# Kernel tuning notes

Measured on AMD Instinct MI355X. Metric: run time of the kernel, lower is better.

## Reference

```python
import jax, jax.numpy as jnp
import numpy as np

B, N, T = 512, 24, 25
IN, L, H, OUT = 8, 64, 256, 128


def quat_mul(q, r):
    w1, x1, y1, z1 = jnp.split(q, 4, -1)
    w2, x2, y2, z2 = jnp.split(r, 4, -1)
    return jnp.concatenate([
        w1 * w2 - x1 * x2 - y1 * y2 - z1 * z2,
        w1 * x2 + x1 * w2 + y1 * z2 - z1 * y2,
        w1 * y2 - x1 * z2 + y1 * w2 + z1 * x2,
        w1 * z2 + x1 * y2 - y1 * x2 + z1 * w2], -1)


def node_linear(x, W, b, G):
    # per-node weights [N,F,O], then graph-influence mixing G[N,N]
    y = jnp.einsum('bnf,nfo->bno', x, W) + b
    return jnp.einsum('mn,bno->bmo', G, y)


def graph_linear(x, W, b, G):
    # shared weights [F,O], then graph-influence mixing
    y = jnp.einsum('bnf,fo->bno', x, W) + b
    return jnp.einsum('mn,bno->bmo', G, y)


def lstm_step(x, h, c, Wx, Wh, b, G):
    gates = jnp.einsum('bnf,nfo->bno', x, Wx) + jnp.einsum('bnf,nfo->bno', h, Wh) + b
    gates = jnp.einsum('mn,bno->bmo', G, gates)
    i, f, g, o = jnp.split(gates, 4, -1)
    c = jax.nn.sigmoid(f) * c + jax.nn.sigmoid(i) * jnp.tanh(g)
    h = jax.nn.sigmoid(o) * jnp.tanh(c)
    return h, c


def _p(key, shape, scale):
    return jax.random.normal(key, shape, jnp.float32) * scale


def setup_inputs() -> dict:
    key = jax.random.key(0)
    ks = jax.random.split(key, 20)
    in0 = L + IN
    inp = {
        'x': jax.random.normal(ks[0], (B, 1, N, IN), jnp.float32),
        'enc': jax.random.normal(ks[1], (B, 1, N, H), jnp.float32),
        'z': jax.random.normal(ks[2], (B, 1, N, L), jnp.float32),
        'y': jax.random.normal(ks[3], (B, T, N, 4), jnp.float32),
        'G': jnp.eye(N, dtype=jnp.float32) + 0.02 * jax.random.normal(ks[4], (N, N), jnp.float32),
        'Wx0': _p(ks[5], (N, in0, 4 * OUT), in0 ** -0.5),
        'Wh0': _p(ks[6], (N, OUT, 4 * OUT), OUT ** -0.5),
        'b0': jnp.zeros((N, 4 * OUT), jnp.float32),
        'Wx1': _p(ks[7], (N, OUT, 4 * OUT), OUT ** -0.5),
        'Wh1': _p(ks[8], (N, OUT, 4 * OUT), OUT ** -0.5),
        'b1': jnp.zeros((N, 4 * OUT), jnp.float32),
        'fc_W': _p(ks[9], (N, OUT, OUT), OUT ** -0.5),
        'fc_b': jnp.zeros((N, OUT), jnp.float32),
        'fc2_W': _p(ks[10], (N, OUT, OUT), OUT ** -0.5),
        'fc2_b': jnp.zeros((N, OUT), jnp.float32),
        'ih1_W': _p(ks[11], (H, OUT), H ** -0.5),
        'ih1_b': jnp.zeros((OUT,), jnp.float32),
        'ih2_W': _p(ks[12], (H, OUT), H ** -0.5),
        'ih2_b': jnp.zeros((OUT,), jnp.float32),
        'loc_W': _p(ks[13], (OUT, 3), OUT ** -0.5),
        'loc_b': jnp.zeros((3,), jnp.float32),
        'logz_W': _p(ks[14], (OUT, 4), OUT ** -0.5),
        'logz_b': jnp.zeros((4,), jnp.float32),
    }
    return inp


def reference(x, enc, z, y, G, Wx0, Wh0, b0, Wx1, Wh1, b1, fc_W, fc_b, fc2_W, fc2_b,
              ih1_W, ih1_b, ih2_W, ih2_b, loc_W, loc_b, logz_W, logz_b):
    # eval mode: dropout = identity, no teacher forcing (y unused); rnn2/xi2 are dead code.
    xs, zs, encs = x[:, 0], z[:, 0], enc[:, 0]          # [B,N,*]
    h0 = graph_linear(encs, ih1_W, ih1_b, G)            # shared initial h for both layers
    c0 = graph_linear(encs, ih2_W, ih2_b, G)            # shared initial c for both layers
    loc_start0 = xs[..., :4]
    xi0 = jnp.concatenate([zs, xs], -1)                 # [B,N,L+IN]

    def step(carry, _):
        xi, loc_start, h1, c1, h2, c2 = carry
        h1, c1 = lstm_step(xi, h1, c1, Wx0, Wh0, b0, G)
        h2, c2 = lstm_step(h1, h2, c2, Wx1, Wh1, b1, G)
        yi = jnp.tanh(h2)
        yi1 = jnp.tanh(node_linear(yi, fc_W, fc_b, G))
        yi2 = jnp.tanh(node_linear(yi, fc2_W, fc2_b, G))
        loc3 = graph_linear(yi1, loc_W, loc_b, G)       # [B,N,3]
        log_Z = graph_linear(yi2, logz_W, logz_b, G)    # [B,N,4]
        w = jnp.ones(loc3.shape[:-1] + (1,), loc3.dtype)
        loc4 = jnp.concatenate([w, loc3], -1)
        loc_d = loc4 * jax.lax.rsqrt(jnp.sum(loc4 * loc4, -1, keepdims=True))  # validate
        loc = quat_mul(loc_start, loc_d)                # state_representation.sum
        xi_next = jnp.concatenate([zs, loc, loc_d], -1)
        return (xi_next, loc, h1, c1, h2, c2), (loc, log_Z)

    _, (locs, logzs) = jax.lax.scan(step, (xi0, loc_start0, h0, c0, h0, c0), None, length=T)
    out = jnp.moveaxis(locs, 0, 1)[:, :, None]          # [B,T,1,N,4]
    out_log_diag = jnp.moveaxis(logzs, 0, 1)[:, :, None]
    return out, out_log_diag
```

## Files before the change

kernel.cpp:

```cpp
#include <hip/hip_runtime.h>
#include <math.h>

#define Bsz 512
#define Nn  24
#define Tt  25

typedef _Float16 f16;
typedef _Float16 f16x8 __attribute__((ext_vector_type(8)));
typedef _Float16 f16x4 __attribute__((ext_vector_type(4)));
typedef float f32x4 __attribute__((ext_vector_type(4)));

__global__ __launch_bounds__(256) void gemm128(
    const f16* __restrict__ Act, const float* __restrict__ Act32, int Ka,
    const f16* __restrict__ W, size_t wstride, int otiles, int bpn,
    const float* __restrict__ bias, int bstride,
    f16* __restrict__ Y, int ystride, int yoff)
{
    const int bid = blockIdx.x;
    const int n     = (bid & 7) + 8 * (bid / (8 * bpn));
    const int inner = (bid >> 3) % bpn;
    const int o0 = (inner % otiles) * 128;
    const int b0 = (inner / otiles) * 128;
    const int tid  = threadIdx.x;
    const int wave = tid >> 6, lane = tid & 63;
    const int wm = (wave >> 1) * 64;
    const int wn = (wave & 1) * 64;
    const int m16 = lane & 15, quad = lane >> 4;

    __shared__ __attribute__((aligned(16))) f16 sW[128][72];
    __shared__ __attribute__((aligned(16))) f16 sB[128][72];

    const f16* Wn = W + (size_t)n * wstride;
    f32x4 acc[4][4] = {};
    const int r = tid >> 3, cc = (tid & 7) * 8;

    for (int k0 = 0; k0 < Ka; k0 += 64) {
        for (int row = r; row < 128; row += 32)
            *(f16x8*)&sW[row][cc] = *(const f16x8*)&Wn[(size_t)(o0 + row) * Ka + k0 + cc];
        if (Act) {
            for (int row = r; row < 128; row += 32)
                *(f16x8*)&sB[row][cc] = *(const f16x8*)&Act[((size_t)(b0 + row) * Nn + n) * Ka + k0 + cc];
        } else {
            for (int row = r; row < 128; row += 32) {
                const float* src = &Act32[((size_t)(b0 + row) * Nn + n) * Ka + k0 + cc];
                f16x8 v;
#pragma unroll
                for (int u = 0; u < 8; u++) v[u] = (f16)src[u];
                *(f16x8*)&sB[row][cc] = v;
            }
        }
        __syncthreads();
#pragma unroll
        for (int kk = 0; kk < 64; kk += 32) {
            f16x8 af[4], bf[4];
#pragma unroll
            for (int i = 0; i < 4; i++)
                af[i] = *(const f16x8*)&sW[wm + i * 16 + m16][kk + quad * 8];
#pragma unroll
            for (int j = 0; j < 4; j++)
                bf[j] = *(const f16x8*)&sB[wn + j * 16 + m16][kk + quad * 8];
#pragma unroll
            for (int i = 0; i < 4; i++)
#pragma unroll
                for (int j = 0; j < 4; j++)
                    acc[i][j] = __builtin_amdgcn_mfma_f32_16x16x32_f16(af[i], bf[j], acc[i][j], 0, 0, 0);
        }
        __syncthreads();
    }
#pragma unroll
    for (int i = 0; i < 4; i++) {
        const int orow = o0 + wm + i * 16 + quad * 4;
        float4 bv = make_float4(0.f, 0.f, 0.f, 0.f);
        if (bias) bv = *(const float4*)&bias[(size_t)n * bstride + orow];
#pragma unroll
        for (int j = 0; j < 4; j++) {
            const int bcol = b0 + wn + j * 16 + m16;
            size_t yi = ((size_t)bcol * Nn + n) * (size_t)ystride + yoff + orow;
            f16x4 o4;
            o4[0] = (f16)(acc[i][j][0] + bv.x);
            o4[1] = (f16)(acc[i][j][1] + bv.y);
            o4[2] = (f16)(acc[i][j][2] + bv.z);
            o4[3] = (f16)(acc[i][j][3] + bv.w);
            *(f16x4*)&Y[yi] = o4;
        }
    }
}

__global__ __launch_bounds__(256) void prep_w01(
    const float* __restrict__ Wx0, const float* __restrict__ Wh0,
    const float* __restrict__ Wx1, const float* __restrict__ Wh1,
    f16* __restrict__ Wz, f16* __restrict__ W2ext, f16* __restrict__ W8,
    f16* __restrict__ Wh0t)
{
    size_t idx = (size_t)blockIdx.x * 256 + threadIdx.x;
    const size_t nz = (size_t)Nn * 512 * 64;
    const size_t n2 = (size_t)Nn * 1024 * 256;
    const size_t n8 = (size_t)Nn * 8 * 512;
    const size_t nh = (size_t)Nn * 512 * 128;
    if (idx < nz) {
        int k = idx & 63; int o = (idx >> 6) & 511; int n = (int)(idx >> 15);
        Wz[idx] = (f16)Wx0[((size_t)n * 72 + k) * 512 + o];
    } else if (idx < nz + n2) {
        size_t i3 = idx - nz;
        int k = (int)(i3 & 255);
        size_t no = i3 >> 8;
        int o = (int)(no & 1023); int n = (int)(no >> 10);
        float v;
        if (o < 512) v = (k < 128) ? Wx1[((size_t)n * 128 + k) * 512 + o]
                                   : Wh1[((size_t)n * 128 + (k - 128)) * 512 + o];
        else         v = (k < 128) ? Wh0[((size_t)n * 128 + k) * 512 + (o - 512)] : 0.f;
        W2ext[i3] = (f16)v;
    } else if (idx < nz + n2 + n8) {
        size_t i4 = idx - nz - n2;
        int o = (int)(i4 & 511);
        size_t ko = i4 >> 9;
        int k = (int)(ko & 7); int n = (int)(ko >> 3);
        W8[i4] = (f16)Wx0[((size_t)n * 72 + 64 + k) * 512 + o];
    } else if (idx < nz + n2 + n8 + nh) {
        size_t i5 = idx - nz - n2 - n8;
        int k = (int)(i5 & 127);
        size_t no = i5 >> 7;
        int o = (int)(no & 511); int n = (int)(no >> 9);
        Wh0t[i5] = (f16)Wh0[((size_t)n * 128 + k) * 512 + o];
    }
}

__global__ __launch_bounds__(256) void prep_wf(
    const float* __restrict__ fcW, const float* __restrict__ fc2W,
    f16* __restrict__ Wtf)
{
    size_t idx = (size_t)blockIdx.x * 256 + threadIdx.x;
    if (idx >= (size_t)Nn * 256 * 128) return;
    int k = (int)(idx & 127);
    size_t no = idx >> 7;
    int o = (int)(no & 255); int n = (int)(no >> 8);
    float v = (o < 128) ? fcW[((size_t)n * 128 + k) * 128 + o]
                        : fc2W[((size_t)n * 128 + k) * 128 + (o - 128)];
    Wtf[idx] = (f16)v;
}

__global__ __launch_bounds__(256) void prep_wi(
    const float* __restrict__ ih1W, const float* __restrict__ ih2W,
    const float* __restrict__ ih1b, const float* __restrict__ ih2b,
    const float* __restrict__ fcb, const float* __restrict__ fc2b,
    const float* __restrict__ b1,
    f16* __restrict__ Wti, float* __restrict__ bi, float* __restrict__ bcat,
    float* __restrict__ bcat2)
{
    int idx = blockIdx.x * 256 + threadIdx.x;
    int k = idx & 255, o = idx >> 8;
    Wti[idx] = (f16)((o < 128) ? ih1W[(size_t)k * 128 + o] : ih2W[(size_t)k * 128 + (o - 128)]);
    if (idx < 256) bi[idx] = (idx < 128) ? ih1b[idx] : ih2b[idx - 128];
    if (idx < Nn * 256) {
        int n = idx >> 8, oo = idx & 255;
        bcat[idx] = (oo < 128) ? fcb[n * 128 + oo] : fc2b[n * 128 + (oo - 128)];
    }
    if (idx < Nn * 1024) {
        int n = idx >> 10, oo = idx & 1023;
        bcat2[idx] = (oo < 512) ? b1[n * 512 + oo] : 0.f;
    }
}

__global__ __launch_bounds__(256) void init_small(
    const float* __restrict__ x, f16* __restrict__ v8f, float* __restrict__ ls)
{
    size_t idx = (size_t)blockIdx.x * 256 + threadIdx.x;
    if (idx < (size_t)Bsz * Nn * 8) {
        v8f[idx] = (f16)x[idx];
        if ((idx & 7) < 4) {
            size_t bn = idx >> 3;
            ls[bn * 4 + (idx & 3)] = x[idx];
        }
    }
}

__global__ __launch_bounds__(256) void mix_init(
    const f16* __restrict__ Yhc, const float* __restrict__ G,
    f16* __restrict__ h0f, f16* __restrict__ l2cat,
    float* __restrict__ c1, float* __restrict__ c2)
{
    const int b = blockIdx.x;
    const int tid = threadIdx.x;
    __shared__ float sY[6144], sG[576];
    for (int i = tid; i < 576; i += 256) sG[i] = G[i];
    for (int v = tid; v < 768; v += 256) {
        int c8 = (v & 31) * 8, n = v >> 5;
        f16x8 t = *(const f16x8*)&Yhc[((size_t)b * Nn + n) * 256 + c8];
        float* d = &sY[n * 256 + c8];
#pragma unroll
        for (int u = 0; u < 8; u++) d[u] = (float)t[u];
    }
    __syncthreads();
    for (int w = tid; w < 3072; w += 256) {
        int o = w & 127, m = w >> 7;
        float ah = 0.f, ac = 0.f;
#pragma unroll
        for (int n = 0; n < 24; n++) {
            float g = sG[m * 24 + n];
            ah += g * sY[n * 256 + o];
            ac += g * sY[n * 256 + 128 + o];
        }
        size_t row = (size_t)b * Nn + m;
        f16 hf = (f16)ah;
        h0f[row * 128 + o] = hf;
        l2cat[row * 256 + 128 + o] = hf;
        c1[row * 128 + o] = ac;
        c2[row * 128 + o] = ac;
    }
}

__global__ __launch_bounds__(256) void mix1c(
    const f16* __restrict__ ypB, const f16* __restrict__ base1,
    const f16* __restrict__ W8, const f16* __restrict__ v8f,
    const float* __restrict__ G,
    float* __restrict__ c1, f16* __restrict__ l2cat)
{
    const int bg = blockIdx.x >> 2;
    const int jt = (blockIdx.x & 3) * 32;
    const int b0 = bg * 8;
    const int tid = threadIdx.x;
    __shared__ __attribute__((aligned(16))) f16 sYc[8][24][136];
    __shared__ float sG[576];
    __shared__ __attribute__((aligned(16))) f16 sV8[8][24][8];
    for (int i = tid; i < 576; i += 256) sG[i] = G[i];
    for (int i = tid; i < 192; i += 256) {
        int bb = i / 24, n = i - bb * 24;
        *(f16x8*)&sV8[bb][n][0] = *(const f16x8*)&v8f[((size_t)(b0 + bb) * Nn + n) * 8];
    }
    __syncthreads();
    for (int i = tid; i < 3072; i += 256) {
        const int c8 = (i & 15) * 8;
        const int n  = (i >> 4) % 24;
        const int bb = (i >> 4) / 24;
        const int g = c8 >> 5;
        const int o8 = g * 128 + jt + (c8 & 31);
        const size_t rowb = (size_t)(b0 + bb) * Nn + n;
        f16x8 pp = *(const f16x8*)&ypB[rowb * 1024 + 512 + o8];
        f16x8 bs = *(const f16x8*)&base1[rowb * 512 + o8];
        float acc[8];
#pragma unroll
        for (int u = 0; u < 8; u++) acc[u] = (float)pp[u] + (float)bs[u];
#pragma unroll
        for (int k = 0; k < 8; k++) {
            float v = (float)sV8[bb][n][k];
            f16x8 ww = *(const f16x8*)&W8[((size_t)n * 8 + k) * 512 + o8];
#pragma unroll
            for (int u = 0; u < 8; u++) acc[u] += v * (float)ww[u];
        }
        f16x8 oo;
#pragma unroll
        for (int u = 0; u < 8; u++) oo[u] = (f16)acc[u];
        *(f16x8*)&sYc[bb][n][c8] = oo;
    }
    __syncthreads();
    for (int w = tid; w < 1536; w += 256) {
        const int j4 = (w & 7) * 4;
        const int m  = (w >> 3) % 24;
        const int bb = (w >> 3) / 24;
        float gi[4] = {}, gf[4] = {}, gg[4] = {}, go[4] = {};
        const float* gr = &sG[m * 24];
#pragma unroll
        for (int n = 0; n < 24; n++) {
            float g = gr[n];
            const f16* yn = &sYc[bb][n][0];
            f16x4 vi = *(const f16x4*)&yn[j4];
            f16x4 vf = *(const f16x4*)&yn[32 + j4];
            f16x4 vg = *(const f16x4*)&yn[64 + j4];
            f16x4 vo = *(const f16x4*)&yn[96 + j4];
#pragma unroll
            for (int u = 0; u < 4; u++) {
                gi[u] += g * (float)vi[u];
                gf[u] += g * (float)vf[u];
                gg[u] += g * (float)vg[u];
                go[u] += g * (float)vo[u];
            }
        }
        const size_t row = (size_t)(b0 + bb) * Nn + m;
        const int col = jt + j4;
        float cv[4];
        *(float4*)cv = *(const float4*)&c1[row * 128 + col];
        f16x4 ha;
#pragma unroll
        for (int u = 0; u < 4; u++) {
            float si = 1.f / (1.f + expf(-gi[u]));
            float sf = 1.f / (1.f + expf(-gf[u]));
            float so = 1.f / (1.f + expf(-go[u]));
            float cn = sf * cv[u] + si * tanhf(gg[u]);
            cv[u] = cn;
            ha[u] = (f16)(so * tanhf(cn));
        }
        *(float4*)&c1[row * 128 + col] = *(float4*)cv;
        *(f16x4*)&l2cat[row * 256 + col] = ha;
    }
}

__global__ __launch_bounds__(256) void mix2(
    const f16* __restrict__ ypB, const float* __restrict__ G,
    float* __restrict__ c,
    f16* __restrict__ dstA, f16* __restrict__ dstB)
{
    const int b = blockIdx.x;
    const int tid = threadIdx.x;
    __shared__ __attribute__((aligned(16))) f16 sY[12288];
    __shared__ float sG[576];
    for (int i = tid; i < 576; i += 256) sG[i] = G[i];
    for (int i = tid; i < 1536; i += 256) {
        int n = i >> 6, c8 = (i & 63) * 8;
        *(f16x8*)&sY[n * 512 + c8] = *(const f16x8*)&ypB[((size_t)b * Nn + n) * 1024 + c8];
    }
    __syncthreads();
    for (int w = tid; w < 768; w += 256) {
        const int m = w >> 5, j4 = (w & 31) * 4;
        float gi[4] = {}, gf[4] = {}, gg[4] = {}, go[4] = {};
        const float* gr = &sG[m * 24];
#pragma unroll
        for (int n = 0; n < 24; n++) {
            float g = gr[n];
            const f16* yn = &sY[n * 512];
            f16x4 vi = *(const f16x4*)&yn[j4];
            f16x4 vf = *(const f16x4*)&yn[128 + j4];
            f16x4 vg = *(const f16x4*)&yn[256 + j4];
            f16x4 vo = *(const f16x4*)&yn[384 + j4];
#pragma unroll
            for (int u = 0; u < 4; u++) {
                gi[u] += g * (float)vi[u];
                gf[u] += g * (float)vf[u];
                gg[u] += g * (float)vg[u];
                go[u] += g * (float)vo[u];
            }
        }
        const size_t row = (size_t)b * Nn + m;
        float cv[4];
        *(float4*)cv = *(const float4*)&c[row * 128 + j4];
        f16x4 ha, hb;
#pragma unroll
        for (int u = 0; u < 4; u++) {
            float si = 1.f / (1.f + expf(-gi[u]));
            float sf = 1.f / (1.f + expf(-gf[u]));
            float so = 1.f / (1.f + expf(-go[u]));
            float cn = sf * cv[u] + si * tanhf(gg[u]);
            cv[u] = cn;
            float h = so * tanhf(cn);
            ha[u] = (f16)h;
            hb[u] = (f16)tanhf(h);
        }
        *(float4*)&c[row * 128 + j4] = *(float4*)cv;
        *(f16x4*)&dstA[row * 256 + 128 + j4] = ha;
        *(f16x4*)&dstB[row * 128 + j4] = hb;
    }
}

__global__ __launch_bounds__(256) void finstep(
    const f16* __restrict__ p, const float* __restrict__ G,
    const float* __restrict__ locW, const float* __restrict__ locb,
    const float* __restrict__ lzW, const float* __restrict__ lzb,
    float* __restrict__ ls, f16* __restrict__ v8f,
    float* __restrict__ out, int t)
{
    const int b = blockIdx.x;
    const int tid = threadIdx.x;
    __shared__ __attribute__((aligned(16))) f16 sP[6144];
    __shared__ __attribute__((aligned(16))) f16 sY1[3072], sY2[3072];
    __shared__ float sG[576];
    __shared__ float sLp[24][3], sZp[24][4], sL3[24][3], sZ3[24][4];
    for (int i = tid; i < 576; i += 256) sG[i] = G[i];
    for (int i = tid; i < 768; i += 256) {
        int n = i >> 5, c8 = (i & 31) * 8;
        *(f16x8*)&sP[n * 256 + c8] = *(const f16x8*)&p[((size_t)b * Nn + n) * 256 + c8];
    }
    __syncthreads();
    for (int w = tid; w < 768; w += 256) {
        const int m = w >> 5, o4 = (w & 31) * 4;
        float a1[4] = {}, a2[4] = {};
        const float* gr = &sG[m * 24];
#pragma unroll
        for (int n = 0; n < 24; n++) {
            float g = gr[n];
            f16x4 p1 = *(const f16x4*)&sP[n * 256 + o4];
            f16x4 p2 = *(const f16x4*)&sP[n * 256 + 128 + o4];
#pragma unroll
            for (int u = 0; u < 4; u++) { a1[u] += g * (float)p1[u]; a2[u] += g * (float)p2[u]; }
        }
        f16x4 y1, y2;
#pragma unroll
        for (int u = 0; u < 4; u++) { y1[u] = (f16)tanhf(a1[u]); y2[u] = (f16)tanhf(a2[u]); }
        *(f16x4*)&sY1[m * 128 + o4] = y1;
        *(f16x4*)&sY2[m * 128 + o4] = y2;
    }
    __syncthreads();
    if (tid < 72) {
        int m = tid / 3, j = tid - m * 3;
        float s = locb[j];
        for (int o = 0; o < 128; o++) s += (float)sY1[m * 128 + o] * locW[o * 3 + j];
        sLp[m][j] = s;
    } else if (tid < 168) {
        int w2 = tid - 72; int m = w2 >> 2, j = w2 & 3;
        float s = lzb[j];
        for (int o = 0; o < 128; o++) s += (float)sY2[m * 128 + o] * lzW[o * 4 + j];
        sZp[m][j] = s;
    }
    __syncthreads();
    if (tid < 72) {
        int m = tid / 3, j = tid - m * 3;
        float s = 0.f;
#pragma unroll
        for (int n = 0; n < 24; n++) s += sG[m * 24 + n] * sLp[n][j];
        sL3[m][j] = s;
    } else if (tid < 168) {
        int w2 = tid - 72; int m = w2 >> 2, j = w2 & 3;
        float s = 0.f;
#pragma unroll
        for (int n = 0; n < 24; n++) s += sG[m * 24 + n] * sZp[n][j];
        sZ3[m][j] = s;
    }
    __syncthreads();
    if (tid < 24) {
        const int m = tid;
        float xx = sL3[m][0], xy = sL3[m][1], xz = sL3[m][2];
        float r = rsqrtf(1.f + xx * xx + xy * xy + xz * xz);
        float dw = r, dx = xx * r, dy = xy * r, dz = xz * r;
        size_t li = ((size_t)b * Nn + m) * 4;
        float qw = ls[li], qx = ls[li + 1], qy = ls[li + 2], qz = ls[li + 3];
        float lw = qw * dw - qx * dx - qy * dy - qz * dz;
        float lx = qw * dx + qx * dw + qy * dz - qz * dy;
        float ly = qw * dy - qx * dz + qy * dw + qz * dx;
        float lz = qw * dz + qx * dy - qy * dx + qz * dw;
        size_t oi = (((size_t)b * Tt + t) * Nn + m) * 4;
        out[oi + 0] = lw; out[oi + 1] = lx; out[oi + 2] = ly; out[oi + 3] = lz;
        size_t zi = (size_t)Bsz * Tt * Nn * 4 + oi;
        out[zi + 0] = sZ3[m][0]; out[zi + 1] = sZ3[m][1];
        out[zi + 2] = sZ3[m][2]; out[zi + 3] = sZ3[m][3];
        ls[li] = lw; ls[li + 1] = lx; ls[li + 2] = ly; ls[li + 3] = lz;
        f16x8 v8;
        v8[0] = (f16)lw; v8[1] = (f16)lx; v8[2] = (f16)ly; v8[3] = (f16)lz;
        v8[4] = (f16)dw; v8[5] = (f16)dx; v8[6] = (f16)dy; v8[7] = (f16)dz;
        *(f16x8*)&v8f[((size_t)b * Nn + m) * 8] = v8;
    }
}

extern "C" void kernel_launch(void* const* d_in, const int* in_sizes, int n_in,
                              void* d_out, int out_size, void* d_ws, size_t ws_size,
                              hipStream_t stream)
{
    const float* x    = (const float*)d_in[0];
    const float* enc  = (const float*)d_in[1];
    const float* z    = (const float*)d_in[2];
    const float* G    = (const float*)d_in[4];
    const float* Wx0  = (const float*)d_in[5];
    const float* Wh0  = (const float*)d_in[6];
    const float* b0i  = (const float*)d_in[7];
    const float* Wx1  = (const float*)d_in[8];
    const float* Wh1  = (const float*)d_in[9];
    const float* b1i  = (const float*)d_in[10];
    const float* fcW  = (const float*)d_in[11];
    const float* fcb  = (const float*)d_in[12];
    const float* fc2W = (const float*)d_in[13];
    const float* fc2b = (const float*)d_in[14];
    const float* ih1W = (const float*)d_in[15];
    const float* ih1b = (const float*)d_in[16];
    const float* ih2W = (const float*)d_in[17];
    const float* ih2b = (const float*)d_in[18];
    const float* locW = (const float*)d_in[19];
    const float* locb = (const float*)d_in[20];
    const float* lzW  = (const float*)d_in[21];
    const float* lzb  = (const float*)d_in[22];
    float* out = (float*)d_out;

    const size_t BN = (size_t)Bsz * Nn;
    char* wp = (char*)d_ws;
    size_t off = 0;
    auto carve = [&](size_t bytes) -> char* {
        char* pc = wp + off;
        off += (bytes + 255) & ~(size_t)255;
        return pc;
    };
    f16*   Wz     = (f16*)carve((size_t)Nn * 512 * 64 * 2);
    f16*   W2ext  = (f16*)carve((size_t)Nn * 1024 * 256 * 2);
    f16*   W8     = (f16*)carve((size_t)Nn * 8 * 512 * 2);
    f16*   Wh0t   = (f16*)carve((size_t)Nn * 512 * 128 * 2);
    f16*   Wtf    = (f16*)carve((size_t)Nn * 256 * 128 * 2);
    f16*   Wti    = (f16*)carve((size_t)256 * 256 * 2);
    float* bcat   = (float*)carve((size_t)Nn * 256 * 4);
    float* bcat2  = (float*)carve((size_t)Nn * 1024 * 4);
    float* bi     = (float*)carve(256 * 4);
    f16*   base1  = (f16*)carve(BN * 512 * 2);
    f16*   l2cat  = (f16*)carve(BN * 256 * 2);
    f16*   yib    = (f16*)carve(BN * 128 * 2);
    f16*   h0f    = (f16*)carve(BN * 128 * 2);
    float* c1     = (float*)carve(BN * 128 * 4);
    float* c2     = (float*)carve(BN * 128 * 4);
    float* ls     = (float*)carve(BN * 4 * 4);
    f16*   v8f    = (f16*)carve(BN * 8 * 2);
    f16*   ypB    = (f16*)carve(BN * 1024 * 2);
    f16*   yp0    = (f16*)carve(BN * 256 * 2);
    f16*   pbuf   = (f16*)carve(BN * 256 * 2);

    prep_w01<<<34176, 256, 0, stream>>>(Wx0, Wh0, Wx1, Wh1, Wz, W2ext, W8, Wh0t);
    prep_wf<<<3072, 256, 0, stream>>>(fcW, fc2W, Wtf);
    prep_wi<<<256, 256, 0, stream>>>(ih1W, ih2W, ih1b, ih2b, fcb, fc2b, b1i,
                                     Wti, bi, bcat, bcat2);
    init_small<<<384, 256, 0, stream>>>(x, v8f, ls);

    gemm128<<<384, 256, 0, stream>>>(nullptr, z, 64, Wz, (size_t)512 * 64, 4, 16,
                                     b0i, 512, base1, 512, 0);
    gemm128<<<192, 256, 0, stream>>>(nullptr, enc, 256, Wti, 0, 2, 8,
                                     bi, 0, yp0, 256, 0);
    mix_init<<<512, 256, 0, stream>>>(yp0, G, h0f, l2cat, c1, c2);
    gemm128<<<384, 256, 0, stream>>>(h0f, nullptr, 128, Wh0t, (size_t)512 * 128, 4, 16,
                                     nullptr, 0, ypB, 1024, 512);

    for (int t = 0; t < Tt; t++) {
        mix1c<<<256, 256, 0, stream>>>(ypB, base1, W8, v8f, G, c1, l2cat);
        gemm128<<<768, 256, 0, stream>>>(l2cat, nullptr, 256, W2ext, (size_t)1024 * 256,
                                         8, 32, bcat2, 1024, ypB, 1024, 0);
        mix2<<<512, 256, 0, stream>>>(ypB, G, c2, l2cat, yib);
        gemm128<<<192, 256, 0, stream>>>(yib, nullptr, 128, Wtf, (size_t)256 * 128,
                                         2, 8, bcat, 256, pbuf, 256, 0);
        finstep<<<512, 256, 0, stream>>>(pbuf, G, locW, locb, lzW, lzb, ls, v8f, out, t);
    }
}
```

Before: 2.698 ms.

## Fold z-projection into recurrent GEMM by extending K to 320 and tiled weight prep

The constant z input is appended to the activation buffer (l2cat now 320 wide), and the matching Wx0 rows are added to the Wh0 half of the extended weight. This removes the separate base1 precompute and its per-step load in mix1c, and the layer-0 bias moves into bcat2. Weight-prep kernels are rewritten as tiled shared-memory transposes for coalesced access, and the initial h0 GEMM reuses the extended weights. In exchange, every per-step GEMM does 25% more K work, including a Wx1/Wh1 half that multiplies the z columns by zero weights.

```diff
diff --git a/kernel.cpp b/kernel.cpp
--- a/kernel.cpp
+++ b/kernel.cpp
@@ -12,14 +12,14 @@
 
 __global__ __launch_bounds__(256) void gemm128(
     const f16* __restrict__ Act, const float* __restrict__ Act32, int Ka,
-    const f16* __restrict__ W, size_t wstride, int otiles, int bpn,
+    const f16* __restrict__ W, size_t wstride, int otiles, int bpn, int obase,
     const float* __restrict__ bias, int bstride,
-    f16* __restrict__ Y, int ystride, int yoff)
+    f16* __restrict__ Y, int ystride)
 {
     const int bid = blockIdx.x;
     const int n     = (bid & 7) + 8 * (bid / (8 * bpn));
     const int inner = (bid >> 3) % bpn;
-    const int o0 = (inner % otiles) * 128;
+    const int o0 = obase + (inner % otiles) * 128;
     const int b0 = (inner / otiles) * 128;
     const int tid  = threadIdx.x;
     const int wave = tid >> 6, lane = tid & 63;
@@ -70,12 +70,11 @@
 #pragma unroll
     for (int i = 0; i < 4; i++) {
         const int orow = o0 + wm + i * 16 + quad * 4;
-        float4 bv = make_float4(0.f, 0.f, 0.f, 0.f);
-        if (bias) bv = *(const float4*)&bias[(size_t)n * bstride + orow];
+        float4 bv = *(const float4*)&bias[(size_t)n * bstride + orow];
 #pragma unroll
         for (int j = 0; j < 4; j++) {
             const int bcol = b0 + wn + j * 16 + m16;
-            size_t yi = ((size_t)bcol * Nn + n) * (size_t)ystride + yoff + orow;
+            size_t yi = ((size_t)bcol * Nn + n) * (size_t)ystride + orow;
             f16x4 o4;
             o4[0] = (f16)(acc[i][j][0] + bv.x);
             o4[1] = (f16)(acc[i][j][1] + bv.y);
@@ -86,70 +85,83 @@
     }
 }
 
-__global__ __launch_bounds__(256) void prep_w01(
+__global__ __launch_bounds__(256) void prep_w2ext(
     const float* __restrict__ Wx0, const float* __restrict__ Wh0,
     const float* __restrict__ Wx1, const float* __restrict__ Wh1,
-    f16* __restrict__ Wz, f16* __restrict__ W2ext, f16* __restrict__ W8,
-    f16* __restrict__ Wh0t)
-{
-    size_t idx = (size_t)blockIdx.x * 256 + threadIdx.x;
-    const size_t nz = (size_t)Nn * 512 * 64;
-    const size_t n2 = (size_t)Nn * 1024 * 256;
-    const size_t n8 = (size_t)Nn * 8 * 512;
-    const size_t nh = (size_t)Nn * 512 * 128;
-    if (idx < nz) {
-        int k = idx & 63; int o = (idx >> 6) & 511; int n = (int)(idx >> 15);
-        Wz[idx] = (f16)Wx0[((size_t)n * 72 + k) * 512 + o];
-    } else if (idx < nz + n2) {
-        size_t i3 = idx - nz;
-        int k = (int)(i3 & 255);
-        size_t no = i3 >> 8;
-        int o = (int)(no & 1023); int n = (int)(no >> 10);
-        float v;
-        if (o < 512) v = (k < 128) ? Wx1[((size_t)n * 128 + k) * 512 + o]
-                                   : Wh1[((size_t)n * 128 + (k - 128)) * 512 + o];
-        else         v = (k < 128) ? Wh0[((size_t)n * 128 + k) * 512 + (o - 512)] : 0.f;
-        W2ext[i3] = (f16)v;
-    } else if (idx < nz + n2 + n8) {
-        size_t i4 = idx - nz - n2;
-        int o = (int)(i4 & 511);
-        size_t ko = i4 >> 9;
-        int k = (int)(ko & 7); int n = (int)(ko >> 3);
-        W8[i4] = (f16)Wx0[((size_t)n * 72 + 64 + k) * 512 + o];
-    } else if (idx < nz + n2 + n8 + nh) {
-        size_t i5 = idx - nz - n2 - n8;
-        int k = (int)(i5 & 127);
-        size_t no = i5 >> 7;
-        int o = (int)(no & 511); int n = (int)(no >> 9);
-        Wh0t[i5] = (f16)Wh0[((size_t)n * 128 + k) * 512 + o];
-    }
-}
-
-__global__ __launch_bounds__(256) void prep_wf(
+    f16* __restrict__ W2ext)
+{
+    const int bid = blockIdx.x;
+    const int kt = bid % 5, ot = (bid / 5) % 16, n = bid / 80;
+    const int k0 = kt * 64, o0 = ot * 64;
+    const int tid = threadIdx.x;
+    __shared__ f16 sT[64][72];
+    const int tc = tid & 63, tr = tid >> 6;
+#pragma unroll
+    for (int i = 0; i < 16; i++) {
+        const int kk = k0 + i * 4 + tr;
+        const int oo = o0 + tc;
+        float v = 0.f;
+        if (oo < 512) {
+            if (kk < 128)      v = Wx1[((size_t)n * 128 + kk) * 512 + oo];
+            else if (kk < 256) v = Wh1[((size_t)n * 128 + (kk - 128)) * 512 + oo];
+        } else {
+            if (kk < 128)      v = Wh0[((size_t)n * 128 + kk) * 512 + (oo - 512)];
+            else if (kk >= 256) v = Wx0[((size_t)n * 72 + (kk - 256)) * 512 + (oo - 512)];
+        }
+        sT[i * 4 + tr][tc] = (f16)v;
+    }
+    __syncthreads();
+#pragma unroll
+    for (int i = 0; i < 16; i++) {
+        const int oo = i * 4 + tr;
+        W2ext[((size_t)n * 1024 + o0 + oo) * 320 + k0 + tc] = sT[tc][oo];
+    }
+}
+
+__global__ __launch_bounds__(256) void prep_wtf(
     const float* __restrict__ fcW, const float* __restrict__ fc2W,
     f16* __restrict__ Wtf)
 {
-    size_t idx = (size_t)blockIdx.x * 256 + threadIdx.x;
-    if (idx >= (size_t)Nn * 256 * 128) return;
-    int k = (int)(idx & 127);
-    size_t no = idx >> 7;
-    int o = (int)(no & 255); int n = (int)(no >> 8);
-    float v = (o < 128) ? fcW[((size_t)n * 128 + k) * 128 + o]
-                        : fc2W[((size_t)n * 128 + k) * 128 + (o - 128)];
-    Wtf[idx] = (f16)v;
-}
-
-__global__ __launch_bounds__(256) void prep_wi(
+    const int bid = blockIdx.x;
+    const int kt = bid & 1, ot = (bid >> 1) & 3, n = bid >> 3;
+    const int k0 = kt * 64, o0 = ot * 64;
+    const int tid = threadIdx.x;
+    __shared__ f16 sT[64][72];
+    const int tc = tid & 63, tr = tid >> 6;
+#pragma unroll
+    for (int i = 0; i < 16; i++) {
+        const int kk = k0 + i * 4 + tr, oo = o0 + tc;
+        float v = (oo < 128) ? fcW[((size_t)n * 128 + kk) * 128 + oo]
+                             : fc2W[((size_t)n * 128 + kk) * 128 + (oo - 128)];
+        sT[i * 4 + tr][tc] = (f16)v;
+    }
+    __syncthreads();
+#pragma unroll
+    for (int i = 0; i < 16; i++) {
+        const int oo = i * 4 + tr;
+        Wtf[((size_t)n * 256 + o0 + oo) * 128 + k0 + tc] = sT[tc][oo];
+    }
+}
+
+__global__ __launch_bounds__(256) void prep_small(
+    const float* __restrict__ Wx0,
     const float* __restrict__ ih1W, const float* __restrict__ ih2W,
     const float* __restrict__ ih1b, const float* __restrict__ ih2b,
     const float* __restrict__ fcb, const float* __restrict__ fc2b,
-    const float* __restrict__ b1,
-    f16* __restrict__ Wti, float* __restrict__ bi, float* __restrict__ bcat,
-    float* __restrict__ bcat2)
+    const float* __restrict__ b0w, const float* __restrict__ b1w,
+    f16* __restrict__ W8, f16* __restrict__ Wti,
+    float* __restrict__ bi, float* __restrict__ bcat, float* __restrict__ bcat2)
 {
     int idx = blockIdx.x * 256 + threadIdx.x;
-    int k = idx & 255, o = idx >> 8;
-    Wti[idx] = (f16)((o < 128) ? ih1W[(size_t)k * 128 + o] : ih2W[(size_t)k * 128 + (o - 128)]);
+    if (idx < Nn * 8 * 512) {
+        int o = idx & 511; int ko = idx >> 9;
+        int k = ko & 7, n = ko >> 3;
+        W8[idx] = (f16)Wx0[((size_t)n * 72 + 64 + k) * 512 + o];
+    }
+    if (idx < 65536) {
+        int k = idx & 255, o = idx >> 8;
+        Wti[idx] = (f16)((o < 128) ? ih1W[(size_t)k * 128 + o] : ih2W[(size_t)k * 128 + (o - 128)]);
+    }
     if (idx < 256) bi[idx] = (idx < 128) ? ih1b[idx] : ih2b[idx - 128];
     if (idx < Nn * 256) {
         int n = idx >> 8, oo = idx & 255;
@@ -157,14 +169,20 @@
     }
     if (idx < Nn * 1024) {
         int n = idx >> 10, oo = idx & 1023;
-        bcat2[idx] = (oo < 512) ? b1[n * 512 + oo] : 0.f;
-    }
-}
-
-__global__ __launch_bounds__(256) void init_small(
-    const float* __restrict__ x, f16* __restrict__ v8f, float* __restrict__ ls)
+        bcat2[idx] = (oo < 512) ? b1w[n * 512 + oo] : b0w[n * 512 + (oo - 512)];
+    }
+}
+
+__global__ __launch_bounds__(256) void init_zl(
+    const float* __restrict__ x, const float* __restrict__ z,
+    f16* __restrict__ l2cat, f16* __restrict__ v8f, float* __restrict__ ls)
 {
     size_t idx = (size_t)blockIdx.x * 256 + threadIdx.x;
+    if (idx < (size_t)Bsz * Nn * 64) {
+        size_t bn = idx >> 6;
+        int j = (int)(idx & 63);
+        l2cat[bn * 320 + 256 + j] = (f16)z[bn * 64 + j];
+    }
     if (idx < (size_t)Bsz * Nn * 8) {
         v8f[idx] = (f16)x[idx];
         if ((idx & 7) < 4) {
@@ -176,8 +194,7 @@
 
 __global__ __launch_bounds__(256) void mix_init(
     const f16* __restrict__ Yhc, const float* __restrict__ G,
-    f16* __restrict__ h0f, f16* __restrict__ l2cat,
-    float* __restrict__ c1, float* __restrict__ c2)
+    f16* __restrict__ l2cat, float* __restrict__ c1, float* __restrict__ c2)
 {
     const int b = blockIdx.x;
     const int tid = threadIdx.x;
@@ -202,17 +219,16 @@
         }
         size_t row = (size_t)b * Nn + m;
         f16 hf = (f16)ah;
-        h0f[row * 128 + o] = hf;
-        l2cat[row * 256 + 128 + o] = hf;
+        l2cat[row * 320 + o] = hf;
+        l2cat[row * 320 + 128 + o] = hf;
         c1[row * 128 + o] = ac;
         c2[row * 128 + o] = ac;
     }
 }
 
 __global__ __launch_bounds__(256) void mix1c(
-    const f16* __restrict__ ypB, const f16* __restrict__ base1,
-    const f16* __restrict__ W8, const f16* __restrict__ v8f,
-    const float* __restrict__ G,
+    const f16* __restrict__ ypB, const f16* __restrict__ W8,
+    const f16* __restrict__ v8f, const float* __restrict__ G,
     float* __restrict__ c1, f16* __restrict__ l2cat)
 {
     const int bg = blockIdx.x >> 2;
@@ -236,10 +252,9 @@
         const int o8 = g * 128 + jt + (c8 & 31);
         const size_t rowb = (size_t)(b0 + bb) * Nn + n;
         f16x8 pp = *(const f16x8*)&ypB[rowb * 1024 + 512 + o8];
-        f16x8 bs = *(const f16x8*)&base1[rowb * 512 + o8];
         float acc[8];
 #pragma unroll
-        for (int u = 0; u < 8; u++) acc[u] = (float)pp[u] + (float)bs[u];
+        for (int u = 0; u < 8; u++) acc[u] = (float)pp[u];
 #pragma unroll
         for (int k = 0; k < 8; k++) {
             float v = (float)sV8[bb][n][k];
@@ -290,14 +305,13 @@
             ha[u] = (f16)(so * tanhf(cn));
         }
         *(float4*)&c1[row * 128 + col] = *(float4*)cv;
-        *(f16x4*)&l2cat[row * 256 + col] = ha;
+        *(f16x4*)&l2cat[row * 320 + col] = ha;
     }
 }
 
 __global__ __launch_bounds__(256) void mix2(
     const f16* __restrict__ ypB, const float* __restrict__ G,
-    float* __restrict__ c,
-    f16* __restrict__ dstA, f16* __restrict__ dstB)
+    float* __restrict__ c, f16* __restrict__ l2cat, f16* __restrict__ yib)
 {
     const int b = blockIdx.x;
     const int tid = threadIdx.x;
@@ -345,8 +359,8 @@
             hb[u] = (f16)tanhf(h);
         }
         *(float4*)&c[row * 128 + j4] = *(float4*)cv;
-        *(f16x4*)&dstA[row * 256 + 128 + j4] = ha;
-        *(f16x4*)&dstB[row * 128 + j4] = hb;
+        *(f16x4*)&l2cat[row * 320 + 128 + j4] = ha;
+        *(f16x4*)&yib[row * 128 + j4] = hb;
     }
 }
 
@@ -474,19 +488,15 @@
         off += (bytes + 255) & ~(size_t)255;
         return pc;
     };
-    f16*   Wz     = (f16*)carve((size_t)Nn * 512 * 64 * 2);
-    f16*   W2ext  = (f16*)carve((size_t)Nn * 1024 * 256 * 2);
+    f16*   W2ext  = (f16*)carve((size_t)Nn * 1024 * 320 * 2);
     f16*   W8     = (f16*)carve((size_t)Nn * 8 * 512 * 2);
-    f16*   Wh0t   = (f16*)carve((size_t)Nn * 512 * 128 * 2);
     f16*   Wtf    = (f16*)carve((size_t)Nn * 256 * 128 * 2);
     f16*   Wti    = (f16*)carve((size_t)256 * 256 * 2);
     float* bcat   = (float*)carve((size_t)Nn * 256 * 4);
     float* bcat2  = (float*)carve((size_t)Nn * 1024 * 4);
     float* bi     = (float*)carve(256 * 4);
-    f16*   base1  = (f16*)carve(BN * 512 * 2);
-    f16*   l2cat  = (f16*)carve(BN * 256 * 2);
+    f16*   l2cat  = (f16*)carve(BN * 320 * 2);
     f16*   yib    = (f16*)carve(BN * 128 * 2);
-    f16*   h0f    = (f16*)carve(BN * 128 * 2);
     float* c1     = (float*)carve(BN * 128 * 4);
     float* c2     = (float*)carve(BN * 128 * 4);
     float* ls     = (float*)carve(BN * 4 * 4);
@@ -495,27 +505,25 @@
     f16*   yp0    = (f16*)carve(BN * 256 * 2);
     f16*   pbuf   = (f16*)carve(BN * 256 * 2);
 
-    prep_w01<<<34176, 256, 0, stream>>>(Wx0, Wh0, Wx1, Wh1, Wz, W2ext, W8, Wh0t);
-    prep_wf<<<3072, 256, 0, stream>>>(fcW, fc2W, Wtf);
-    prep_wi<<<256, 256, 0, stream>>>(ih1W, ih2W, ih1b, ih2b, fcb, fc2b, b1i,
-                                     Wti, bi, bcat, bcat2);
-    init_small<<<384, 256, 0, stream>>>(x, v8f, ls);
-
-    gemm128<<<384, 256, 0, stream>>>(nullptr, z, 64, Wz, (size_t)512 * 64, 4, 16,
-                                     b0i, 512, base1, 512, 0);
-    gemm128<<<192, 256, 0, stream>>>(nullptr, enc, 256, Wti, 0, 2, 8,
-                                     bi, 0, yp0, 256, 0);
-    mix_init<<<512, 256, 0, stream>>>(yp0, G, h0f, l2cat, c1, c2);
-    gemm128<<<384, 256, 0, stream>>>(h0f, nullptr, 128, Wh0t, (size_t)512 * 128, 4, 16,
-                                     nullptr, 0, ypB, 1024, 512);
+    prep_w2ext<<<1920, 256, 0, stream>>>(Wx0, Wh0, Wx1, Wh1, W2ext);
+    prep_wtf<<<192, 256, 0, stream>>>(fcW, fc2W, Wtf);
+    prep_small<<<384, 256, 0, stream>>>(Wx0, ih1W, ih2W, ih1b, ih2b, fcb, fc2b,
+                                        b0i, b1i, W8, Wti, bi, bcat, bcat2);
+    init_zl<<<3072, 256, 0, stream>>>(x, z, l2cat, v8f, ls);
+
+    gemm128<<<192, 256, 0, stream>>>(nullptr, enc, 256, Wti, 0, 2, 8, 0,
+                                     bi, 0, yp0, 256);
+    mix_init<<<512, 256, 0, stream>>>(yp0, G, l2cat, c1, c2);
+    gemm128<<<384, 256, 0, stream>>>(l2cat, nullptr, 320, W2ext, (size_t)1024 * 320,
+                                     4, 16, 512, bcat2, 1024, ypB, 1024);
 
     for (int t = 0; t < Tt; t++) {
-        mix1c<<<256, 256, 0, stream>>>(ypB, base1, W8, v8f, G, c1, l2cat);
-        gemm128<<<768, 256, 0, stream>>>(l2cat, nullptr, 256, W2ext, (size_t)1024 * 256,
-                                         8, 32, bcat2, 1024, ypB, 1024, 0);
+        mix1c<<<256, 256, 0, stream>>>(ypB, W8, v8f, G, c1, l2cat);
+        gemm128<<<768, 256, 0, stream>>>(l2cat, nullptr, 320, W2ext, (size_t)1024 * 320,
+                                         8, 32, 0, bcat2, 1024, ypB, 1024);
         mix2<<<512, 256, 0, stream>>>(ypB, G, c2, l2cat, yib);
         gemm128<<<192, 256, 0, stream>>>(yib, nullptr, 128, Wtf, (size_t)256 * 128,
-                                         2, 8, bcat, 256, pbuf, 256, 0);
+                                         2, 8, 0, bcat, 256, pbuf, 256);
         finstep<<<512, 256, 0, stream>>>(pbuf, G, locW, locb, lzW, lzb, ls, v8f, out, t);
     }
 }
```

New measurement: 2.677 ms. About the same (-0.8%).
